# Kernel optimization log

Hardware: AMD Instinct MI355X
Metric: run time of the kernel (lower is better)

The kernel has to match this reference:

```python
import jax, jax.numpy as jnp
import numpy as np

B, S, D, H = 2, 2048, 1024, 16
DK = D // H  # 64


def setup_inputs() -> dict:
    key = jax.random.key(0)
    ks = jax.random.split(key, 11)
    scale = 1.0 / np.sqrt(D)
    inp = {
        "x": jax.random.normal(ks[0], (B, S, D), dtype=jnp.float32),
        "z": jax.random.normal(ks[1], (B, S, D), dtype=jnp.float32),
        # causal mask, broadcast over batch and heads; masked_fill where mask==0
        "mask": jnp.tril(jnp.ones((1, 1, S, S), dtype=jnp.int32)),
        "wq_w": jax.random.normal(ks[2], (D, D), dtype=jnp.float32) * scale,
        "wq_b": jax.random.normal(ks[3], (D,), dtype=jnp.float32) * 0.01,
        "wk_w": jax.random.normal(ks[4], (D, D), dtype=jnp.float32) * scale,
        "wk_b": jax.random.normal(ks[5], (D,), dtype=jnp.float32) * 0.01,
        "wv_w": jax.random.normal(ks[6], (D, D), dtype=jnp.float32) * scale,
        "wv_b": jax.random.normal(ks[7], (D,), dtype=jnp.float32) * 0.01,
        "wo_w": jax.random.normal(ks[8], (D, D), dtype=jnp.float32) * scale,
        "wo_b": jax.random.normal(ks[9], (D,), dtype=jnp.float32) * 0.01,
    }
    return inp


def reference(x, z, mask, wq_w, wq_b, wk_w, wk_b, wv_w, wv_b, wo_w, wo_b):
    # torch Linear: y = x @ W.T + b
    q = x @ wq_w.T + wq_b
    k = z @ wk_w.T + wk_b
    # NOTE: faithful to source bug: value uses wk, not wv (wv is a dead param)
    v = z @ wk_w.T + wk_b

    def split_heads(t):  # [B,S,D] -> [B,H,S,DK]
        return t.reshape(B, S, H, DK).transpose(0, 2, 1, 3)

    q, k, v = split_heads(q), split_heads(k), split_heads(v)

    scores = jnp.einsum("bhqd,bhkd->bhqk", q, k) * (DK ** -0.5)
    scores = jnp.where(mask == 0, -jnp.inf, scores)
    attn_weights = jax.nn.softmax(scores, axis=-1)  # [B,H,S,S]
    atn = jnp.einsum("bhqk,bhkd->bhqd", attn_weights, v)

    concat = atn.transpose(0, 2, 1, 3).reshape(B, S, D)
    output = concat @ wo_w.T + wo_b  # dropout rate 0.0 -> identity
    concat_attn_weight = attn_weights.sum(axis=1)  # [B,S,S]
    return output, concat_attn_weight
```

## Files before the change

kernel.cpp:

```cpp
#include <hip/hip_runtime.h>

typedef __bf16 bf16_t;
typedef __bf16 bf16x4 __attribute__((ext_vector_type(4)));
typedef __bf16 bf16x8 __attribute__((ext_vector_type(8)));
typedef float  f32x4  __attribute__((ext_vector_type(4)));

#define MFMA(a, b, c) __builtin_amdgcn_mfma_f32_16x16x32_bf16((a), (b), (c), 0, 0, 0)

static constexpr int Bsz = 2, S = 2048, D = 1024, H = 16, DK = 64;
#define QSCALE 0.18033688011112042f

__global__ __launch_bounds__(256) void cvt5(
    const float* __restrict__ x, const float* __restrict__ z,
    const float* __restrict__ wq, const float* __restrict__ wk,
    const float* __restrict__ wo,
    bf16_t* __restrict__ xb, bf16_t* __restrict__ zb,
    bf16_t* __restrict__ wqb, bf16_t* __restrict__ wkb, bf16_t* __restrict__ wob)
{
    constexpr int NXZ = Bsz * S * D / 4;
    constexpr int NW  = D * D / 4;
    int i = blockIdx.x * 256 + threadIdx.x;
    const float* s; bf16_t* d; int off;
    if (i < NXZ)                 { s = x;  d = xb;  off = i; }
    else if (i < 2 * NXZ)        { s = z;  d = zb;  off = i - NXZ; }
    else if (i < 2 * NXZ + NW)   { s = wq; d = wqb; off = i - 2 * NXZ; }
    else if (i < 2 * NXZ + 2*NW) { s = wk; d = wkb; off = i - 2 * NXZ - NW; }
    else                         { s = wo; d = wob; off = i - 2 * NXZ - 2 * NW; }
    float4 v = *(const float4*)&s[(size_t)off * 4];
    bf16x4 o;
    o[0] = (bf16_t)v.x; o[1] = (bf16_t)v.y; o[2] = (bf16_t)v.z; o[3] = (bf16_t)v.w;
    *(bf16x4*)&d[(size_t)off * 4] = o;
}

__global__ __launch_bounds__(512) void gemm_qk(
    const bf16_t* __restrict__ xA, const bf16_t* __restrict__ wqB,
    const float* __restrict__ wqb, bf16_t* __restrict__ Qc,
    const bf16_t* __restrict__ zA, const bf16_t* __restrict__ wkB,
    const float* __restrict__ wkb, bf16_t* __restrict__ Kc,
    bf16_t* __restrict__ KTout)
{
    constexpr int N = D, K = D;
    const int zi = blockIdx.z;
    const bf16_t* A    = zi ? zA  : xA;
    const bf16_t* B    = zi ? wkB : wqB;
    const float*  bias = zi ? wkb : wqb;
    bf16_t*       C    = zi ? Kc  : Qc;
    const float   sc   = zi ? 1.f : QSCALE;

    __shared__ bf16_t As[2][128][40];
    __shared__ bf16_t Bs[2][128][40];

    const int t    = threadIdx.x;
    const int wave = t >> 6, lane = t & 63;
    const int quad = lane >> 4, l15 = lane & 15;
    const int wm = (wave >> 1) * 32, wn = (wave & 1) * 64;
    const int rowbase = blockIdx.y * 128, colbase = blockIdx.x * 128;
    const int r  = t >> 2;
    const int cc = (t & 3) << 3;

    f32x4 acc[2][4];
#pragma unroll
    for (int i = 0; i < 2; ++i)
#pragma unroll
        for (int j = 0; j < 4; ++j) acc[i][j] = {0.f, 0.f, 0.f, 0.f};

    bf16x8 areg = *(const bf16x8*)&A[(size_t)(rowbase + r) * K + cc];
    bf16x8 breg = *(const bf16x8*)&B[(size_t)(colbase + r) * K + cc];
    *(bf16x8*)&As[0][r][cc] = areg;
    *(bf16x8*)&Bs[0][r][cc] = breg;
    __syncthreads();

    for (int kt = 0; kt < K; kt += 32) {
        const int cur = (kt >> 5) & 1, nxt = cur ^ 1;
        const bool more = (kt + 32) < K;
        if (more) {
            areg = *(const bf16x8*)&A[(size_t)(rowbase + r) * K + kt + 32 + cc];
            breg = *(const bf16x8*)&B[(size_t)(colbase + r) * K + kt + 32 + cc];
        }

        bf16x8 af[2], bfr[4];
#pragma unroll
        for (int mt = 0; mt < 2; ++mt)
            af[mt] = *(const bf16x8*)&As[cur][wm + mt * 16 + l15][quad * 8];
#pragma unroll
        for (int nt = 0; nt < 4; ++nt)
            bfr[nt] = *(const bf16x8*)&Bs[cur][wn + nt * 16 + l15][quad * 8];
        __builtin_amdgcn_s_setprio(1);
#pragma unroll
        for (int mt = 0; mt < 2; ++mt)
#pragma unroll
            for (int nt = 0; nt < 4; ++nt)
                acc[mt][nt] = MFMA(af[mt], bfr[nt], acc[mt][nt]);
        __builtin_amdgcn_s_setprio(0);

        if (more) {
            *(bf16x8*)&As[nxt][r][cc] = areg;
            *(bf16x8*)&Bs[nxt][r][cc] = breg;
        }
        __syncthreads();
    }

#pragma unroll
    for (int nt = 0; nt < 4; ++nt) {
        int col  = colbase + wn + nt * 16 + l15;
        float bv = bias[col];
#pragma unroll
        for (int mt = 0; mt < 2; ++mt) {
            int row0 = rowbase + wm + mt * 16 + quad * 4;
#pragma unroll
            for (int rr = 0; rr < 4; ++rr) {
                float v = (acc[mt][nt][rr] + bv) * sc;
                C[(size_t)(row0 + rr) * N + col] = (bf16_t)v;
                if (zi) {
                    int row = row0 + rr;
                    int bb = row >> 11, srow = row & (S - 1);
                    int hh = col >> 6,  dd   = col & 63;
                    KTout[(((size_t)bb * H + hh) * DK + dd) * S + srow] = (bf16_t)v;
                }
            }
        }
    }
}

__global__ __launch_bounds__(256) void gemm_obt(
    const bf16_t* __restrict__ A, const bf16_t* __restrict__ B,
    const float* __restrict__ bias, float* __restrict__ C)
{
    constexpr int N = D, K = D;
    __shared__ bf16_t As[2][64][40];
    __shared__ bf16_t Bs[2][128][40];

    const int t    = threadIdx.x;
    const int wave = t >> 6, lane = t & 63;
    const int quad = lane >> 4, l15 = lane & 15;
    const int wm = (wave >> 1) * 32, wn = (wave & 1) * 64;
    const int rowbase = blockIdx.y * 64, colbase = blockIdx.x * 128;
    const int r  = t >> 2;
    const int cc = (t & 3) << 3;

    f32x4 acc[2][4];
#pragma unroll
    for (int i = 0; i < 2; ++i)
#pragma unroll
        for (int j = 0; j < 4; ++j) acc[i][j] = {0.f, 0.f, 0.f, 0.f};

    bf16x8 areg = *(const bf16x8*)&A[(size_t)(rowbase + r) * K + cc];
    bf16x8 breg0 = *(const bf16x8*)&B[(size_t)(colbase + r) * K + cc];
    bf16x8 breg1 = *(const bf16x8*)&B[(size_t)(colbase + 64 + r) * K + cc];
    *(bf16x8*)&As[0][r][cc]      = areg;
    *(bf16x8*)&Bs[0][r][cc]      = breg0;
    *(bf16x8*)&Bs[0][64 + r][cc] = breg1;
    __syncthreads();

    for (int kt = 0; kt < K; kt += 32) {
        const int cur = (kt >> 5) & 1, nxt = cur ^ 1;
        const bool more = (kt + 32) < K;
        if (more) {
            areg  = *(const bf16x8*)&A[(size_t)(rowbase + r) * K + kt + 32 + cc];
            breg0 = *(const bf16x8*)&B[(size_t)(colbase + r) * K + kt + 32 + cc];
            breg1 = *(const bf16x8*)&B[(size_t)(colbase + 64 + r) * K + kt + 32 + cc];
        }

        bf16x8 af[2], bfr[4];
#pragma unroll
        for (int mt = 0; mt < 2; ++mt)
            af[mt] = *(const bf16x8*)&As[cur][wm + mt * 16 + l15][quad * 8];
#pragma unroll
        for (int nt = 0; nt < 4; ++nt)
            bfr[nt] = *(const bf16x8*)&Bs[cur][wn + nt * 16 + l15][quad * 8];
        __builtin_amdgcn_s_setprio(1);
#pragma unroll
        for (int mt = 0; mt < 2; ++mt)
#pragma unroll
            for (int nt = 0; nt < 4; ++nt)
                acc[mt][nt] = MFMA(af[mt], bfr[nt], acc[mt][nt]);
        __builtin_amdgcn_s_setprio(0);

        if (more) {
            *(bf16x8*)&As[nxt][r][cc]      = areg;
            *(bf16x8*)&Bs[nxt][r][cc]      = breg0;
            *(bf16x8*)&Bs[nxt][64 + r][cc] = breg1;
        }
        __syncthreads();
    }

#pragma unroll
    for (int nt = 0; nt < 4; ++nt) {
        int col  = colbase + wn + nt * 16 + l15;
        float bv = bias[col];
#pragma unroll
        for (int mt = 0; mt < 2; ++mt) {
            int row0 = rowbase + wm + mt * 16 + quad * 4;
#pragma unroll
            for (int rr = 0; rr < 4; ++rr)
                C[(size_t)(row0 + rr) * N + col] = acc[mt][nt][rr] + bv;
        }
    }
}

__global__ __launch_bounds__(256) void attn_flash(
    const bf16_t* __restrict__ Q, const bf16_t* __restrict__ Km,
    const bf16_t* __restrict__ KT,
    bf16_t* __restrict__ Oc, float* __restrict__ m_ws, float* __restrict__ il_ws)
{
    const int h = blockIdx.y, b = blockIdx.z;
    const int t = threadIdx.x;
    const int wave = t >> 6, lane = t & 63;
    const int quad = lane >> 4, l15 = lane & 15;

    __shared__ bf16_t Ks[2][64][72];
    __shared__ bf16_t KTs[2][64][72];
    __shared__ bf16_t PQ[64][72];

    const int hcol = h * DK;
    const bf16_t* KTh = KT + ((size_t)(b * H + h)) * DK * S;
    const size_t bS = (size_t)b * S;

    const int jr = (t >> 3);
    const int ce = (t & 7) * 8;
    const int iloc = wave * 16 + l15;

    for (int half = 0; half < 2; ++half) {
        const int qt = half == 0 ? (int)blockIdx.x : 31 - (int)blockIdx.x;
        const size_t qrow0 = bS + (size_t)qt * 64;

        __syncthreads();
        bf16x8 qld[2], kreg[2], ktreg[2];
#pragma unroll
        for (int p = 0; p < 2; ++p) {
            qld[p]   = *(const bf16x8*)&Q[(qrow0 + p * 32 + jr) * D + hcol + ce];
            kreg[p]  = *(const bf16x8*)&Km[(bS + p * 32 + jr) * D + hcol + ce];
            ktreg[p] = *(const bf16x8*)&KTh[(size_t)(p * 32 + jr) * S + ce];
        }
#pragma unroll
        for (int p = 0; p < 2; ++p) {
            *(bf16x8*)&PQ[p * 32 + jr][ce]     = qld[p];
            *(bf16x8*)&Ks[0][p * 32 + jr][ce]  = kreg[p];
            *(bf16x8*)&KTs[0][p * 32 + jr][ce] = ktreg[p];
        }
        __syncthreads();
        const bf16x8 qf0 = *(const bf16x8*)&PQ[wave * 16 + l15][quad * 8];
        const bf16x8 qf1 = *(const bf16x8*)&PQ[wave * 16 + l15][32 + quad * 8];

        f32x4 accO[4];
#pragma unroll
        for (int u = 0; u < 4; ++u) accO[u] = {0.f, 0.f, 0.f, 0.f};
        float m_cur = -1e30f, l_cur = 0.f;

        auto softmax_pv = [&](f32x4 sv[4], int cur) {
            float tm = sv[0][0];
#pragma unroll
            for (int nt = 0; nt < 4; ++nt)
#pragma unroll
                for (int r = 0; r < 4; ++r) tm = fmaxf(tm, sv[nt][r]);
            tm = fmaxf(tm, __shfl_xor(tm, 16));
            tm = fmaxf(tm, __shfl_xor(tm, 32));
            if (__any(tm > m_cur + 8.f)) {
                float m_new = fmaxf(m_cur, tm);
                float alpha = exp2f(m_cur - m_new);
                m_cur = m_new;
                l_cur *= alpha;
                float alpha4[4];
#pragma unroll
                for (int r = 0; r < 4; ++r)
                    alpha4[r] = __shfl(alpha, (quad << 4) + quad * 4 + r, 64);
#pragma unroll
                for (int u = 0; u < 4; ++u)
#pragma unroll
                    for (int r = 0; r < 4; ++r) accO[u][r] *= alpha4[r];
            }
            float rs = 0.f;
#pragma unroll
            for (int nt = 0; nt < 4; ++nt)
#pragma unroll
                for (int r = 0; r < 4; ++r) {
                    float p = exp2f(sv[nt][r] - m_cur);
                    sv[nt][r] = p;
                    rs += p;
                }
            rs += __shfl_xor(rs, 16);
            rs += __shfl_xor(rs, 32);
            l_cur += rs;

#pragma unroll
            for (int nt = 0; nt < 4; ++nt) {
                bf16x4 pk;
                pk[0] = (bf16_t)sv[nt][0]; pk[1] = (bf16_t)sv[nt][1];
                pk[2] = (bf16_t)sv[nt][2]; pk[3] = (bf16_t)sv[nt][3];
                *(bf16x4*)&PQ[wave * 16 + l15][nt * 16 + quad * 4] = pk;
            }
            asm volatile("s_waitcnt lgkmcnt(0)" ::: "memory");

            bf16x8 pa0 = *(const bf16x8*)&PQ[wave * 16 + l15][quad * 8];
            bf16x8 pa1 = *(const bf16x8*)&PQ[wave * 16 + l15][32 + quad * 8];
            __builtin_amdgcn_s_setprio(1);
#pragma unroll
            for (int u = 0; u < 4; ++u) {
                bf16x8 v0 = *(const bf16x8*)&KTs[cur][u * 16 + l15][quad * 8];
                bf16x8 v1 = *(const bf16x8*)&KTs[cur][u * 16 + l15][32 + quad * 8];
                accO[u] = MFMA(pa0, v0, accO[u]);
                accO[u] = MFMA(pa1, v1, accO[u]);
            }
            __builtin_amdgcn_s_setprio(0);
        };

        for (int jt = 0; jt < qt; ++jt) {
            const int cur = jt & 1, nxt = cur ^ 1;
#pragma unroll
            for (int p = 0; p < 2; ++p) {
                kreg[p]  = *(const bf16x8*)&Km[(bS + (size_t)(jt + 1) * 64 + p * 32 + jr) * D + hcol + ce];
                ktreg[p] = *(const bf16x8*)&KTh[(size_t)(p * 32 + jr) * S + (size_t)(jt + 1) * 64 + ce];
            }

            f32x4 sv[4];
            __builtin_amdgcn_s_setprio(1);
#pragma unroll
            for (int nt = 0; nt < 4; ++nt) {
                bf16x8 a0 = *(const bf16x8*)&Ks[cur][nt * 16 + l15][quad * 8];
                bf16x8 a1 = *(const bf16x8*)&Ks[cur][nt * 16 + l15][32 + quad * 8];
                f32x4 a = {0.f, 0.f, 0.f, 0.f};
                a = MFMA(a0, qf0, a);
                a = MFMA(a1, qf1, a);
                sv[nt] = a;
            }
            __builtin_amdgcn_s_setprio(0);
            softmax_pv(sv, cur);

#pragma unroll
            for (int p = 0; p < 2; ++p) {
                *(bf16x8*)&Ks[nxt][p * 32 + jr][ce]  = kreg[p];
                *(bf16x8*)&KTs[nxt][p * 32 + jr][ce] = ktreg[p];
            }
            __syncthreads();
        }

        {
            const int cur = qt & 1;
            f32x4 sv[4];
            __builtin_amdgcn_s_setprio(1);
#pragma unroll
            for (int nt = 0; nt < 4; ++nt) {
                bf16x8 a0 = *(const bf16x8*)&Ks[cur][nt * 16 + l15][quad * 8];
                bf16x8 a1 = *(const bf16x8*)&Ks[cur][nt * 16 + l15][32 + quad * 8];
                f32x4 a = {0.f, 0.f, 0.f, 0.f};
                a = MFMA(a0, qf0, a);
                a = MFMA(a1, qf1, a);
#pragma unroll
                for (int r = 0; r < 4; ++r)
                    if ((nt * 16 + quad * 4 + r) > iloc) a[r] = -1e30f;
                sv[nt] = a;
            }
            __builtin_amdgcn_s_setprio(0);
            softmax_pv(sv, cur);
        }

        float invl = 1.f / l_cur;
        float invl4[4];
#pragma unroll
        for (int r = 0; r < 4; ++r)
            invl4[r] = __shfl(invl, (quad << 4) + quad * 4 + r, 64);
#pragma unroll
        for (int u = 0; u < 4; ++u)
#pragma unroll
            for (int r = 0; r < 4; ++r)
                Oc[(qrow0 + wave * 16 + quad * 4 + r) * D + hcol + u * 16 + l15] =
                    (bf16_t)(accO[u][r] * invl4[r]);

        if (quad == 0) {
            size_t sb = ((size_t)(b * H + h)) * S + (size_t)qt * 64 + wave * 16 + l15;
            m_ws[sb]  = m_cur;
            il_ws[sb] = invl;
        }
    }
}

__global__ __launch_bounds__(256) void attn_wsum(
    const bf16_t* __restrict__ Q, const bf16_t* __restrict__ Km,
    const float* __restrict__ m_ws, const float* __restrict__ il_ws,
    float* __restrict__ out2)
{
    const int jt = blockIdx.x, qt = blockIdx.y, b = blockIdx.z;
    const int t  = threadIdx.x;
    float* tile = out2 + (size_t)b * S * S + (size_t)qt * 64 * S + (size_t)jt * 64;

    if (jt > qt) {
        int r0 = t >> 2, c0 = (t & 3) * 16;
#pragma unroll
        for (int e = 0; e < 16; ++e) tile[(size_t)r0 * S + c0 + e] = 0.f;
        return;
    }

    const int wave = t >> 6, lane = t & 63;
    const int quad = lane >> 4, l15 = lane & 15;
    __shared__ bf16_t Ks[2][64][72];
    __shared__ bf16_t Qs[2][64][72];

    const int jr = (t >> 3), ce = (t & 7) * 8;
    const size_t krow = (size_t)b * S + (size_t)jt * 64;
    const size_t qrow = (size_t)b * S + (size_t)qt * 64;

    f32x4 accs[4];
#pragma unroll
    for (int nt = 0; nt < 4; ++nt) accs[nt] = {0.f, 0.f, 0.f, 0.f};

    bf16x8 kreg[2], qreg[2];
#pragma unroll
    for (int p = 0; p < 2; ++p) {
        kreg[p] = *(const bf16x8*)&Km[(krow + p * 32 + jr) * D + ce];
        qreg[p] = *(const bf16x8*)&Q[(qrow + p * 32 + jr) * D + ce];
    }
#pragma unroll
    for (int p = 0; p < 2; ++p) {
        *(bf16x8*)&Ks[0][p * 32 + jr][ce] = kreg[p];
        *(bf16x8*)&Qs[0][p * 32 + jr][ce] = qreg[p];
    }
    __syncthreads();

    for (int h = 0; h < H; ++h) {
        const int cur = h & 1, nxt = cur ^ 1;

        if (h < H - 1) {
            const int hc = (h + 1) * DK;
#pragma unroll
            for (int p = 0; p < 2; ++p) {
                kreg[p] = *(const bf16x8*)&Km[(krow + p * 32 + jr) * D + hc + ce];
                qreg[p] = *(const bf16x8*)&Q[(qrow + p * 32 + jr) * D + hc + ce];
            }
        }

        bf16x8 qf0 = *(const bf16x8*)&Qs[cur][wave * 16 + l15][quad * 8];
        bf16x8 qf1 = *(const bf16x8*)&Qs[cur][wave * 16 + l15][32 + quad * 8];

        size_t mlb = ((size_t)(b * H + h)) * S + (size_t)qt * 64 + wave * 16 + quad * 4;
        f32x4 mr = *(const f32x4*)&m_ws[mlb];
        f32x4 il = *(const f32x4*)&il_ws[mlb];

#pragma unroll
        for (int nt = 0; nt < 4; ++nt) {
            bf16x8 k0 = *(const bf16x8*)&Ks[cur][nt * 16 + l15][quad * 8];
            bf16x8 k1 = *(const bf16x8*)&Ks[cur][nt * 16 + l15][32 + quad * 8];
            f32x4 a = {0.f, 0.f, 0.f, 0.f};
            __builtin_amdgcn_s_setprio(1);
            a = MFMA(qf0, k0, a);
            a = MFMA(qf1, k1, a);
            __builtin_amdgcn_s_setprio(0);
#pragma unroll
            for (int r = 0; r < 4; ++r) {
                int i = qt * 64 + wave * 16 + quad * 4 + r;
                int j = jt * 64 + nt * 16 + l15;
                float p = (j <= i) ? exp2f(a[r] - mr[r]) * il[r] : 0.f;
                accs[nt][r] += p;
            }
        }

        if (h < H - 1) {
#pragma unroll
            for (int p = 0; p < 2; ++p) {
                *(bf16x8*)&Ks[nxt][p * 32 + jr][ce] = kreg[p];
                *(bf16x8*)&Qs[nxt][p * 32 + jr][ce] = qreg[p];
            }
        }
        __syncthreads();
    }

#pragma unroll
    for (int nt = 0; nt < 4; ++nt)
#pragma unroll
        for (int r = 0; r < 4; ++r)
            tile[(size_t)(wave * 16 + quad * 4 + r) * S + nt * 16 + l15] = accs[nt][r];
}

extern "C" void kernel_launch(void* const* d_in, const int* in_sizes, int n_in,
                              void* d_out, int out_size, void* d_ws, size_t ws_size,
                              hipStream_t stream)
{
    const float* x    = (const float*)d_in[0];
    const float* z    = (const float*)d_in[1];
    const float* wq_w = (const float*)d_in[3];
    const float* wq_b = (const float*)d_in[4];
    const float* wk_w = (const float*)d_in[5];
    const float* wk_b = (const float*)d_in[6];
    const float* wo_w = (const float*)d_in[9];
    const float* wo_b = (const float*)d_in[10];

    float* out  = (float*)d_out;
    float* out2 = out + (size_t)Bsz * S * D;

    float*  m_ws  = (float*)d_ws;
    float*  il_ws = m_ws + (size_t)Bsz * H * S;
    bf16_t* Qws   = (bf16_t*)(il_ws + (size_t)Bsz * H * S);
    bf16_t* Kws   = Qws + (size_t)Bsz * S * D;
    bf16_t* wq_bf = Kws + (size_t)Bsz * S * D;
    bf16_t* wk_bf = wq_bf + (size_t)D * D;
    bf16_t* wo_bf = wk_bf + (size_t)D * D;
    bf16_t* xb    = (bf16_t*)out;
    bf16_t* zb    = xb + (size_t)Bsz * S * D;
    bf16_t* Cc    = (bf16_t*)out2;
    bf16_t* KTws  = Cc + (size_t)Bsz * S * D;

    constexpr int CVT_BLOCKS = (2 * (Bsz * S * D / 4) + 3 * (D * D / 4)) / 256;
    cvt5<<<dim3(CVT_BLOCKS), dim3(256), 0, stream>>>(
        x, z, wq_w, wk_w, wo_w, xb, zb, wq_bf, wk_bf, wo_bf);
    gemm_qk<<<dim3(D / 128, (Bsz * S) / 128, 2), dim3(512), 0, stream>>>(
        xb, wq_bf, wq_b, Qws, zb, wk_bf, wk_b, Kws, KTws);
    attn_flash<<<dim3(S / 128, H, Bsz), dim3(256), 0, stream>>>(
        Qws, Kws, KTws, Cc, m_ws, il_ws);
    gemm_obt<<<dim3(D / 128, (Bsz * S) / 64, 1), dim3(256), 0, stream>>>(
        Cc, wo_bf, wo_b, out);
    attn_wsum<<<dim3(S / 64, S / 64, Bsz), dim3(256), 0, stream>>>(
        Qws, Kws, m_ws, il_ws, out2);
}
```

Before: 274.6 us.

## Load attention-weight-sum fragments directly from global and split off-diagonal tiles

The attn_wsum kernel drops its double-buffered LDS staging of Q and K tiles and loads the MFMA fragments straight from global memory, which removes every __syncthreads in the head loop. Off-diagonal tiles (jt < qt) take a separate path with no causal mask check and fold the scale into an fma. The setprio hints are also removed. The trade-off is that each wave now issues its own uncoalesced, strided global loads, so K fragments are fetched redundantly by all four waves and the kernel depends on cache hits rather than shared-memory reuse.

Result: slower. 369.5 us (+34.5%).

```diff
diff --git a/kernel.cpp b/kernel.cpp
--- a/kernel.cpp
+++ b/kernel.cpp
@@ -392,75 +392,61 @@
 
     const int wave = t >> 6, lane = t & 63;
     const int quad = lane >> 4, l15 = lane & 15;
-    __shared__ bf16_t Ks[2][64][72];
-    __shared__ bf16_t Qs[2][64][72];
-
-    const int jr = (t >> 3), ce = (t & 7) * 8;
+
     const size_t krow = (size_t)b * S + (size_t)jt * 64;
     const size_t qrow = (size_t)b * S + (size_t)qt * 64;
 
+    const bf16_t* qbase = &Q[(qrow + wave * 16 + l15) * D + quad * 8];
+    const bf16_t* kbase = &Km[(krow + l15) * D + quad * 8];
+
     f32x4 accs[4];
 #pragma unroll
     for (int nt = 0; nt < 4; ++nt) accs[nt] = {0.f, 0.f, 0.f, 0.f};
 
-    bf16x8 kreg[2], qreg[2];
-#pragma unroll
-    for (int p = 0; p < 2; ++p) {
-        kreg[p] = *(const bf16x8*)&Km[(krow + p * 32 + jr) * D + ce];
-        qreg[p] = *(const bf16x8*)&Q[(qrow + p * 32 + jr) * D + ce];
-    }
-#pragma unroll
-    for (int p = 0; p < 2; ++p) {
-        *(bf16x8*)&Ks[0][p * 32 + jr][ce] = kreg[p];
-        *(bf16x8*)&Qs[0][p * 32 + jr][ce] = qreg[p];
-    }
-    __syncthreads();
-
-    for (int h = 0; h < H; ++h) {
-        const int cur = h & 1, nxt = cur ^ 1;
-
-        if (h < H - 1) {
-            const int hc = (h + 1) * DK;
-#pragma unroll
-            for (int p = 0; p < 2; ++p) {
-                kreg[p] = *(const bf16x8*)&Km[(krow + p * 32 + jr) * D + hc + ce];
-                qreg[p] = *(const bf16x8*)&Q[(qrow + p * 32 + jr) * D + hc + ce];
-            }
-        }
-
-        bf16x8 qf0 = *(const bf16x8*)&Qs[cur][wave * 16 + l15][quad * 8];
-        bf16x8 qf1 = *(const bf16x8*)&Qs[cur][wave * 16 + l15][32 + quad * 8];
-
-        size_t mlb = ((size_t)(b * H + h)) * S + (size_t)qt * 64 + wave * 16 + quad * 4;
-        f32x4 mr = *(const f32x4*)&m_ws[mlb];
-        f32x4 il = *(const f32x4*)&il_ws[mlb];
-
-#pragma unroll
-        for (int nt = 0; nt < 4; ++nt) {
-            bf16x8 k0 = *(const bf16x8*)&Ks[cur][nt * 16 + l15][quad * 8];
-            bf16x8 k1 = *(const bf16x8*)&Ks[cur][nt * 16 + l15][32 + quad * 8];
-            f32x4 a = {0.f, 0.f, 0.f, 0.f};
-            __builtin_amdgcn_s_setprio(1);
-            a = MFMA(qf0, k0, a);
-            a = MFMA(qf1, k1, a);
-            __builtin_amdgcn_s_setprio(0);
-#pragma unroll
-            for (int r = 0; r < 4; ++r) {
-                int i = qt * 64 + wave * 16 + quad * 4 + r;
-                int j = jt * 64 + nt * 16 + l15;
-                float p = (j <= i) ? exp2f(a[r] - mr[r]) * il[r] : 0.f;
-                accs[nt][r] += p;
-            }
-        }
-
-        if (h < H - 1) {
-#pragma unroll
-            for (int p = 0; p < 2; ++p) {
-                *(bf16x8*)&Ks[nxt][p * 32 + jr][ce] = kreg[p];
-                *(bf16x8*)&Qs[nxt][p * 32 + jr][ce] = qreg[p];
-            }
-        }
-        __syncthreads();
+    const size_t mlb0 = (size_t)(b * H) * S + (size_t)qt * 64 + wave * 16 + quad * 4;
+
+    if (jt < qt) {
+        for (int h = 0; h < H; ++h) {
+            const int hcol = h * DK;
+            bf16x8 qf0 = *(const bf16x8*)&qbase[hcol];
+            bf16x8 qf1 = *(const bf16x8*)&qbase[hcol + 32];
+            f32x4 mr = *(const f32x4*)&m_ws[mlb0 + (size_t)h * S];
+            f32x4 il = *(const f32x4*)&il_ws[mlb0 + (size_t)h * S];
+#pragma unroll
+            for (int nt = 0; nt < 4; ++nt) {
+                bf16x8 k0 = *(const bf16x8*)&kbase[(size_t)nt * 16 * D + hcol];
+                bf16x8 k1 = *(const bf16x8*)&kbase[(size_t)nt * 16 * D + hcol + 32];
+                f32x4 a = {0.f, 0.f, 0.f, 0.f};
+                a = MFMA(qf0, k0, a);
+                a = MFMA(qf1, k1, a);
+#pragma unroll
+                for (int r = 0; r < 4; ++r)
+                    accs[nt][r] = fmaf(exp2f(a[r] - mr[r]), il[r], accs[nt][r]);
+            }
+        }
+    } else {
+        for (int h = 0; h < H; ++h) {
+            const int hcol = h * DK;
+            bf16x8 qf0 = *(const bf16x8*)&qbase[hcol];
+            bf16x8 qf1 = *(const bf16x8*)&qbase[hcol + 32];
+            f32x4 mr = *(const f32x4*)&m_ws[mlb0 + (size_t)h * S];
+            f32x4 il = *(const f32x4*)&il_ws[mlb0 + (size_t)h * S];
+#pragma unroll
+            for (int nt = 0; nt < 4; ++nt) {
+                bf16x8 k0 = *(const bf16x8*)&kbase[(size_t)nt * 16 * D + hcol];
+                bf16x8 k1 = *(const bf16x8*)&kbase[(size_t)nt * 16 * D + hcol + 32];
+                f32x4 a = {0.f, 0.f, 0.f, 0.f};
+                a = MFMA(qf0, k0, a);
+                a = MFMA(qf1, k1, a);
+#pragma unroll
+                for (int r = 0; r < 4; ++r) {
+                    int i = wave * 16 + quad * 4 + r;
+                    int j = nt * 16 + l15;
+                    float p = (j <= i) ? exp2f(a[r] - mr[r]) * il[r] : 0.f;
+                    accs[nt][r] += p;
+                }
+            }
+        }
     }
 
 #pragma unroll
```
